# Kernel optimization log

Hardware: AMD Instinct MI355X
Metric: run time of the kernel (lower is better)

## Reference

```python
import jax, jax.numpy as jnp
import numpy as np

V, E, H, K, L, B = 32000, 512, 1024, 2048, 196, 256


def setup_inputs() -> dict:
    key = jax.random.key(0)
    ks = jax.random.split(key, 16)
    s = 0.02
    return {
        "inputs": jax.random.randint(ks[0], (B, 1), 0, V),
        "hidden": jax.random.normal(ks[1], (B, H), jnp.float32),
        "keys": jax.random.normal(ks[2], (B, L, K), jnp.float32),
        # embedding table
        "emb": jax.random.normal(ks[3], (V, E), jnp.float32) * s,
        # Bahdanau attention: Wq(hidden->H), Wk(keys_hidden->H), v(H->1)
        "Wq": jax.random.normal(ks[4], (H, H), jnp.float32) * s,
        "bq": jnp.zeros((H,), jnp.float32),
        "Wk": jax.random.normal(ks[5], (K, H), jnp.float32) * s,
        "bk": jnp.zeros((H,), jnp.float32),
        "v": jax.random.normal(ks[6], (H, 1), jnp.float32) * s,
        "bv": jnp.zeros((1,), jnp.float32),
        # fc_0: keys_hidden -> hidden
        "fc0_W": jax.random.normal(ks[7], (K, H), jnp.float32) * s,
        "fc0_b": jnp.zeros((H,), jnp.float32),
        # single-layer GRU, input dim E+H (PyTorch layout: [3H, in])
        "W_ih": jax.random.normal(ks[8], (3 * H, E + H), jnp.float32) * s,
        "W_hh": jax.random.normal(ks[9], (3 * H, H), jnp.float32) * s,
        "b_ih": jnp.zeros((3 * H,), jnp.float32),
        "b_hh": jnp.zeros((3 * H,), jnp.float32),
        # fc_1: hidden -> vocab
        "fc1_W": jax.random.normal(ks[10], (H, V), jnp.float32) * s,
        "fc1_b": jnp.zeros((V,), jnp.float32),
    }


def reference(inputs, hidden, keys, emb, Wq, bq, Wk, bk, v, bv,
              fc0_W, fc0_b, W_ih, W_hh, b_ih, b_hh, fc1_W, fc1_b):
    # embedding lookup: [B,1] -> [B,E] (single decode step)
    x = emb[inputs[:, 0]]
    # Bahdanau attention: score = v^T tanh(Wq q + Wk k)
    q = hidden @ Wq + bq                                   # [B,H]
    kproj = jnp.einsum('blk,kh->blh', keys, Wk) + bk        # [B,L,H]
    scores = jnp.tanh(q[:, None, :] + kproj) @ v + bv       # [B,L,1]
    weights = jax.nn.softmax(scores, axis=1)                # [B,L,1]
    context = jnp.sum(weights * keys, axis=1)               # [B,K]
    context = context @ fc0_W + fc0_b                       # [B,H]
    # one GRU step (PyTorch equations)
    rnn_in = jnp.concatenate([x, context], axis=-1)         # [B,E+H]
    gi = rnn_in @ W_ih.T + b_ih                             # [B,3H]
    gh = hidden @ W_hh.T + b_hh                             # [B,3H]
    ir, iz, i_n = jnp.split(gi, 3, axis=-1)
    hr, hz, h_n = jnp.split(gh, 3, axis=-1)
    r = jax.nn.sigmoid(ir + hr)
    z = jax.nn.sigmoid(iz + hz)
    n = jnp.tanh(i_n + r * h_n)
    h_new = (1.0 - z) * n + z * hidden                      # [B,H]
    logits = h_new @ fc1_W + fc1_b                          # [B,V]
    return logits, h_new, weights
```

## Files before the change

### kernel.cpp

```cpp
#include <hip/hip_runtime.h>
#include <cstdint>

#define DEVINL __device__ __forceinline__

typedef __attribute__((ext_vector_type(4))) float floatx4;
typedef __attribute__((ext_vector_type(8))) __bf16 bf16x8;
typedef __attribute__((ext_vector_type(8))) unsigned short ushortx8;
typedef __attribute__((ext_vector_type(4))) unsigned short ushortx4;

DEVINL unsigned short f2bf(float x) {
  unsigned int u = __float_as_uint(x);
  u += 0x7fffu + ((u >> 16) & 1u);
  return (unsigned short)(u >> 16);
}
DEVINL float bf2f(unsigned short u) { return __uint_as_float(((unsigned int)u) << 16); }

DEVINL float fast_tanh(float x) {
  return 1.0f - 2.0f / (__expf(2.0f * x) + 1.0f);
}

DEVINL void gload_lds16(const void* g, void* l) {
  __builtin_amdgcn_global_load_lds(
      (const __attribute__((address_space(1))) void*)g,
      (__attribute__((address_space(3))) void*)l, 16, 0, 0);
}

template <int EPI, bool ABF16, bool XSWZ>
__global__ __launch_bounds__(256) void gemm_bt(
    const float* __restrict__ Af, const unsigned short* __restrict__ Ab, int lda,
    const unsigned short* __restrict__ Bt, int ldb, int Kc,
    float* __restrict__ C, int ldc, int coloff, const float* __restrict__ bias,
    const float* __restrict__ qv, const float* __restrict__ bkv,
    const float* __restrict__ vvec, float* __restrict__ scores, int Lrows, int Hdim)
{
  __shared__ __align__(16) unsigned short As[128 * 32];
  __shared__ __align__(16) unsigned short Bs[128 * 32];

  const int tid  = threadIdx.x;
  const int wave = tid >> 6;
  const int lane = tid & 63;
  const int qd   = lane >> 4;
  const int lm   = lane & 15;
  const int wr   = wave >> 1;
  const int wc   = wave & 1;

  int bx = blockIdx.x, by = blockIdx.y;
  if (XSWZ) {
    const int id = by * 8 + bx;
    const int c = id >> 6, r = id & 63;
    by = c * 8 + (r & 7);
    bx = r >> 3;
  }
  const long n0 = (long)bx * 128;
  const long m0 = (long)by * 128;
  const long k0base = (long)blockIdx.z * Kc;

  floatx4 acc[4][4];
#pragma unroll
  for (int i = 0; i < 4; ++i)
#pragma unroll
    for (int j = 0; j < 4; ++j)
#pragma unroll
      for (int r = 0; r < 4; ++r) acc[i][j][r] = 0.0f;

  const int srow = lane >> 2;
  const int scg  = ((lane & 3) ^ ((lane >> 2) & 3) ^ (lane >> 4)) * 8;
  const int arow = tid >> 1;
  const int q0   = (tid & 1) * 2;
  const int sA   = ((arow & 3) ^ ((arow >> 2) & 3));
  const int fsw  = (qd ^ ((lm ^ (lm >> 2)) & 3)) * 8;

  const int nIter = Kc >> 5;
  for (int it = 0; it < nIter; ++it) {
    const long k0 = k0base + ((long)it << 5);
    {
      const unsigned short* bsrc = Bt + n0 * (size_t)ldb + k0;
#pragma unroll
      for (int q2 = 0; q2 < 2; ++q2) {
        const int rb = wave * 32 + q2 * 16;
        gload_lds16(bsrc + (size_t)(rb + srow) * ldb + scg, &Bs[rb * 32]);
      }
    }
    if (ABF16) {
      const unsigned short* asrc = Ab + m0 * (size_t)lda + k0;
#pragma unroll
      for (int q2 = 0; q2 < 2; ++q2) {
        const int rb = wave * 32 + q2 * 16;
        gload_lds16(asrc + (size_t)(rb + srow) * lda + scg, &As[rb * 32]);
      }
    } else {
      const float* ap = Af + (m0 + arow) * (size_t)lda + k0 + q0 * 8;
      floatx4 f0 = *(const floatx4*)(ap + 0);
      floatx4 f1 = *(const floatx4*)(ap + 4);
      floatx4 f2 = *(const floatx4*)(ap + 8);
      floatx4 f3 = *(const floatx4*)(ap + 12);
      ushortx8 u0, u1;
#pragma unroll
      for (int e = 0; e < 4; ++e) {
        u0[e]     = f2bf(f0[e]);
        u0[e + 4] = f2bf(f1[e]);
        u1[e]     = f2bf(f2[e]);
        u1[e + 4] = f2bf(f3[e]);
      }
      *(ushortx8*)&As[arow * 32 + (q0 ^ sA) * 8]       = u0;
      *(ushortx8*)&As[arow * 32 + ((q0 + 1) ^ sA) * 8] = u1;
    }
    __syncthreads();

    bf16x8 af[4], bfr[4];
#pragma unroll
    for (int i = 0; i < 4; ++i) {
      const int m = wr * 64 + i * 16 + lm;
      af[i] = *(const bf16x8*)&As[m * 32 + fsw];
    }
#pragma unroll
    for (int j = 0; j < 4; ++j) {
      const int n = wc * 64 + j * 16 + lm;
      bfr[j] = *(const bf16x8*)&Bs[n * 32 + fsw];
    }
#pragma unroll
    for (int i = 0; i < 4; ++i)
#pragma unroll
      for (int j = 0; j < 4; ++j)
        acc[i][j] = __builtin_amdgcn_mfma_f32_16x16x32_bf16(af[i], bfr[j], acc[i][j], 0, 0, 0);
    __syncthreads();
  }

  if (EPI == 0) {
#pragma unroll
    for (int j = 0; j < 4; ++j) {
      const long gc = n0 + wc * 64 + j * 16 + lm;
      const float bj = bias[gc];
#pragma unroll
      for (int i = 0; i < 4; ++i) {
        const long gr0 = m0 + wr * 64 + i * 16 + qd * 4;
#pragma unroll
        for (int r = 0; r < 4; ++r)
          C[(gr0 + r) * (size_t)ldc + coloff + gc] = acc[i][j][r] + bj;
      }
    }
  } else if (EPI == 2) {
#pragma unroll
    for (int j = 0; j < 4; ++j) {
      const long gc = n0 + wc * 64 + j * 16 + lm;
      const float bj = (blockIdx.z == 0) ? bias[gc] : 0.0f;
#pragma unroll
      for (int i = 0; i < 4; ++i) {
        const long gr0 = m0 + wr * 64 + i * 16 + qd * 4;
#pragma unroll
        for (int r = 0; r < 4; ++r)
          atomicAdd(&C[(gr0 + r) * (size_t)ldc + coloff + gc], acc[i][j][r] + bj);
      }
    }
  } else {
    float vj[4], bkj[4];
    int gcj[4];
#pragma unroll
    for (int j = 0; j < 4; ++j) {
      gcj[j] = (int)(n0 + wc * 64 + j * 16 + lm);
      vj[j]  = vvec[gcj[j]];
      bkj[j] = bkv[gcj[j]];
    }
    const int m0i = (int)m0;
#pragma unroll
    for (int i = 0; i < 4; ++i) {
#pragma unroll
      for (int r = 0; r < 4; ++r) {
        const int grow = m0i + wr * 64 + i * 16 + qd * 4 + r;
        int brow;
        if (Lrows == 196) brow = (int)((unsigned)(grow * 85599u) >> 24);
        else              brow = grow / Lrows;
        const float* qrow = qv + (size_t)brow * Hdim;
        float s = 0.0f;
#pragma unroll
        for (int j = 0; j < 4; ++j)
          s += fast_tanh(qrow[gcj[j]] + bkj[j] + acc[i][j][r]) * vj[j];
        s += __shfl_xor(s, 1, 64);
        s += __shfl_xor(s, 2, 64);
        s += __shfl_xor(s, 4, 64);
        s += __shfl_xor(s, 8, 64);
        if (lm == 0) atomicAdd(&scores[grow], s);
      }
    }
  }
}

__global__ void transpose_f32_bf16(const float* __restrict__ in,
                                   unsigned short* __restrict__ out, int R, int C) {
  __shared__ float tile[32][33];
  const int c0 = blockIdx.x * 32, r0 = blockIdx.y * 32;
  const int tx = threadIdx.x, ty = threadIdx.y;
#pragma unroll
  for (int yy = 0; yy < 4; ++yy)
    tile[ty + 8 * yy][tx] = in[(size_t)(r0 + ty + 8 * yy) * C + c0 + tx];
  __syncthreads();
#pragma unroll
  for (int yy = 0; yy < 4; ++yy)
    out[(size_t)(c0 + ty + 8 * yy) * R + r0 + tx] = f2bf(tile[tx][ty + 8 * yy]);
}

__global__ void convert_bf16(const float* __restrict__ in,
                             unsigned short* __restrict__ out, int n4) {
  const int idx = blockIdx.x * blockDim.x + threadIdx.x;
  if (idx < n4) {
    floatx4 f = *(const floatx4*)(in + 4 * (size_t)idx);
    ushortx4 u;
#pragma unroll
    for (int e = 0; e < 4; ++e) u[e] = f2bf(f[e]);
    *(ushortx4*)(out + 4 * (size_t)idx) = u;
  }
}

__global__ void gather_emb(const int* __restrict__ inputs, const float* __restrict__ emb,
                           float* __restrict__ rnn_in, int E, int ldr) {
  const int b = blockIdx.x, t = threadIdx.x;
  const int row = inputs[b];
  for (int e = t; e < E; e += 256)
    rnn_in[(size_t)b * ldr + e] = emb[(size_t)row * E + e];
}

__global__ __launch_bounds__(256) void softmax_w(
    const float* __restrict__ scores, const float* __restrict__ bv,
    float* __restrict__ weights, int L)
{
  __shared__ float red[8];
  const int b = blockIdx.x, t = threadIdx.x;
  const int wave = t >> 6;
  float s = (t < L) ? scores[(size_t)b * L + t] + bv[0] : -3.4e38f;
  float m = s;
  for (int o = 32; o > 0; o >>= 1) m = fmaxf(m, __shfl_xor(m, o, 64));
  if ((t & 63) == 0) red[wave] = m;
  __syncthreads();
  m = fmaxf(fmaxf(red[0], red[1]), fmaxf(red[2], red[3]));
  float e = (t < L) ? __expf(s - m) : 0.0f;
  float sum = e;
  for (int o = 32; o > 0; o >>= 1) sum += __shfl_xor(sum, o, 64);
  if ((t & 63) == 0) red[4 + wave] = sum;
  __syncthreads();
  sum = red[4] + red[5] + red[6] + red[7];
  if (t < L) weights[(size_t)b * L + t] = e / sum;
}

template <bool KB16>
__global__ __launch_bounds__(256) void context_k(
    const float* __restrict__ weights, const unsigned short* __restrict__ keys16,
    const float* __restrict__ keysf, float* __restrict__ context, int L, int K)
{
  __shared__ float w[256];
  const int b = blockIdx.x, t = threadIdx.x;
  if (t < L) w[t] = weights[(size_t)b * L + t];
  __syncthreads();
  const int col0 = blockIdx.y * 512 + t * 2;
  float a0 = 0.0f, a1 = 0.0f;
  if (KB16) {
    const unsigned short* kp = keys16 + (size_t)b * L * K + col0;
#pragma unroll 4
    for (int l = 0; l < L; ++l) {
      const unsigned int u = *(const unsigned int*)(kp + (size_t)l * K);
      a0 += w[l] * bf2f((unsigned short)(u & 0xffff));
      a1 += w[l] * bf2f((unsigned short)(u >> 16));
    }
  } else {
    const float* kp = keysf + (size_t)b * L * K + col0;
#pragma unroll 4
    for (int l = 0; l < L; ++l) {
      a0 += w[l] * kp[(size_t)l * K];
      a1 += w[l] * kp[(size_t)l * K + 1];
    }
  }
  context[(size_t)b * K + col0]     = a0;
  context[(size_t)b * K + col0 + 1] = a1;
}

__global__ void gru_kernel(const float* __restrict__ gi, const float* __restrict__ gh,
                           const float* __restrict__ hidden, float* __restrict__ hnew, int H) {
  const int idx = blockIdx.x * blockDim.x + threadIdx.x;
  const int b = idx / H, h = idx % H;
  const size_t base = (size_t)b * 3 * H;
  const float ir = gi[base + h], iz = gi[base + H + h], inn = gi[base + 2 * H + h];
  const float hr = gh[base + h], hz = gh[base + H + h], hn = gh[base + 2 * H + h];
  const float r = 1.0f / (1.0f + __expf(-(ir + hr)));
  const float z = 1.0f / (1.0f + __expf(-(iz + hz)));
  const float n = tanhf(inn + r * hn);
  const float hv = hidden[(size_t)b * H + h];
  hnew[(size_t)b * H + h] = (1.0f - z) * n + z * hv;
}

extern "C" void kernel_launch(void* const* d_in, const int* in_sizes, int n_in,
                              void* d_out, int out_size, void* d_ws, size_t ws_size,
                              hipStream_t stream) {
  constexpr int V = 32000, E = 512, H = 1024, KD = 2048, L = 196, B = 256;
  constexpr int G3 = 3 * H;
  constexpr int EH = E + H;

  const int*   inputs = (const int*)d_in[0];
  const float* hidden = (const float*)d_in[1];
  const float* keys   = (const float*)d_in[2];
  const float* emb    = (const float*)d_in[3];
  const float* Wq     = (const float*)d_in[4];
  const float* bq     = (const float*)d_in[5];
  const float* Wk     = (const float*)d_in[6];
  const float* bk     = (const float*)d_in[7];
  const float* vvec   = (const float*)d_in[8];
  const float* bv     = (const float*)d_in[9];
  const float* fc0_W  = (const float*)d_in[10];
  const float* fc0_b  = (const float*)d_in[11];
  const float* W_ih   = (const float*)d_in[12];
  const float* W_hh   = (const float*)d_in[13];
  const float* b_ih   = (const float*)d_in[14];
  const float* b_hh   = (const float*)d_in[15];
  const float* fc1_W  = (const float*)d_in[16];
  const float* fc1_b  = (const float*)d_in[17];

  float* logits  = (float*)d_out;
  float* hnew    = logits + (size_t)B * V;
  float* weights = hnew + (size_t)B * H;

  char* ws = (char*)d_ws;
  size_t off = 0;
  auto bump = [&off](size_t bytes) {
    size_t p = off;
    off += (bytes + 255) & ~(size_t)255;
    return p;
  };
  unsigned short* WqT   = (unsigned short*)(ws + bump((size_t)H * H * 2));
  unsigned short* WkT   = (unsigned short*)(ws + bump((size_t)H * KD * 2));
  unsigned short* fc0T  = (unsigned short*)(ws + bump((size_t)H * KD * 2));
  unsigned short* fc1T  = (unsigned short*)(ws + bump((size_t)V * H * 2));
  unsigned short* Wih16 = (unsigned short*)(ws + bump((size_t)G3 * EH * 2));
  unsigned short* Whh16 = (unsigned short*)(ws + bump((size_t)G3 * H * 2));
  float* qbuf    = (float*)(ws + bump((size_t)B * H * 4));
  float* scoresb = (float*)(ws + bump((size_t)B * L * 4));
  float* context = (float*)(ws + bump((size_t)B * KD * 4));
  float* rnn_in  = (float*)(ws + bump((size_t)B * EH * 4));
  float* gi      = (float*)(ws + bump((size_t)B * G3 * 4));
  float* gh      = (float*)(ws + bump((size_t)B * G3 * 4));
  unsigned short* keys16 = (unsigned short*)(ws + bump((size_t)B * L * KD * 2));
  const bool useK16 = (off <= ws_size);

  hipMemsetAsync(scoresb, 0, (size_t)B * L * 4, stream);
  hipMemsetAsync(qbuf, 0, (size_t)B * H * 4, stream);
  hipMemsetAsync(rnn_in, 0, (size_t)B * EH * 4, stream);
  hipMemsetAsync(gi, 0, (size_t)B * G3 * 4, stream);
  hipMemsetAsync(gh, 0, (size_t)B * G3 * 4, stream);

  const dim3 tb(32, 8);
  transpose_f32_bf16<<<dim3(H / 32, H / 32), tb, 0, stream>>>(Wq, WqT, H, H);
  transpose_f32_bf16<<<dim3(H / 32, KD / 32), tb, 0, stream>>>(Wk, WkT, KD, H);
  transpose_f32_bf16<<<dim3(H / 32, KD / 32), tb, 0, stream>>>(fc0_W, fc0T, KD, H);
  transpose_f32_bf16<<<dim3(V / 32, H / 32), tb, 0, stream>>>(fc1_W, fc1T, H, V);
  convert_bf16<<<(G3 * EH / 4 + 255) / 256, 256, 0, stream>>>(W_ih, Wih16, G3 * EH / 4);
  convert_bf16<<<(G3 * H / 4 + 255) / 256, 256, 0, stream>>>(W_hh, Whh16, G3 * H / 4);
  if (useK16) {
    const int n4 = B * L * KD / 4;
    convert_bf16<<<(n4 + 255) / 256, 256, 0, stream>>>(keys, keys16, n4);
  }

  gather_emb<<<B, 256, 0, stream>>>(inputs, emb, rnn_in, E, EH);

  gemm_bt<2, false, false><<<dim3(H / 128, B / 128, 4), 256, 0, stream>>>(
      hidden, nullptr, H, WqT, H, H / 4, qbuf, H, 0, bq,
      nullptr, nullptr, nullptr, nullptr, 0, 0);

  if (useK16)
    gemm_bt<1, true, true><<<dim3(H / 128, (B * L) / 128, 1), 256, 0, stream>>>(
        nullptr, keys16, KD, WkT, KD, KD, nullptr, 0, 0, nullptr,
        qbuf, bk, vvec, scoresb, L, H);
  else
    gemm_bt<1, false, true><<<dim3(H / 128, (B * L) / 128, 1), 256, 0, stream>>>(
        keys, nullptr, KD, WkT, KD, KD, nullptr, 0, 0, nullptr,
        qbuf, bk, vvec, scoresb, L, H);

  softmax_w<<<B, 256, 0, stream>>>(scoresb, bv, weights, L);

  if (useK16)
    context_k<true><<<dim3(B, KD / 512), 256, 0, stream>>>(weights, keys16, nullptr,
                                                           context, L, KD);
  else
    context_k<false><<<dim3(B, KD / 512), 256, 0, stream>>>(weights, nullptr, keys,
                                                            context, L, KD);

  gemm_bt<2, false, false><<<dim3(H / 128, B / 128, 4), 256, 0, stream>>>(
      context, nullptr, KD, fc0T, KD, KD / 4, rnn_in, EH, E, fc0_b,
      nullptr, nullptr, nullptr, nullptr, 0, 0);

  gemm_bt<2, false, false><<<dim3(G3 / 128, B / 128, 4), 256, 0, stream>>>(
      rnn_in, nullptr, EH, Wih16, EH, EH / 4, gi, G3, 0, b_ih,
      nullptr, nullptr, nullptr, nullptr, 0, 0);

  gemm_bt<2, false, false><<<dim3(G3 / 128, B / 128, 4), 256, 0, stream>>>(
      hidden, nullptr, H, Whh16, H, H / 4, gh, G3, 0, b_hh,
      nullptr, nullptr, nullptr, nullptr, 0, 0);

  gru_kernel<<<(B * H) / 256, 256, 0, stream>>>(gi, gh, hidden, hnew, H);

  gemm_bt<0, false, false><<<dim3(V / 128, B / 128, 1), 256, 0, stream>>>(
      hnew, nullptr, H, fc1T, H, H, logits, V, 0, fc1_b,
      nullptr, nullptr, nullptr, nullptr, 0, 0);
}
```

Baseline: 1.267 ms.

## Replace key-projection score GEMM with 256x256 eight-phase pipelined MFMA kernel

Adds a dedicated 512-thread kernel for the dominant keys·Wk GEMM with the fused tanh/v score epilogue. It uses 256x256 tiles, double-buffered LDS filled by direct global-to-LDS loads, XOR-swizzled LDS reads, and an eight-phase schedule that interleaves loads with MFMA blocks and raises wave priority around them. The goal is more data reuse per tile and better overlap of memory traffic with matrix math than the previous 128x128 kernel. In exchange it uses a large LDS footprint (128KB) that limits occupancy, hardcodes K=2048, L=196 and H=1024 (batch row is computed by a magic multiply), and still sums scores with atomics.

```diff
diff --git a/kernel.cpp b/kernel.cpp
--- a/kernel.cpp
+++ b/kernel.cpp
@@ -23,6 +23,151 @@
   __builtin_amdgcn_global_load_lds(
       (const __attribute__((address_space(1))) void*)g,
       (__attribute__((address_space(3))) void*)l, 16, 0, 0);
+}
+
+#define SBAR()                          \
+  __builtin_amdgcn_sched_barrier(0);    \
+  __builtin_amdgcn_s_barrier();         \
+  __builtin_amdgcn_sched_barrier(0);
+
+__global__ __launch_bounds__(512) void gemm_scores_8ph(
+    const unsigned short* __restrict__ A, const unsigned short* __restrict__ B,
+    const float* __restrict__ qv, const float* __restrict__ bkv,
+    const float* __restrict__ vvec, float* __restrict__ scores)
+{
+  constexpr int KSH = 2048;
+  constexpr int NT  = 32;
+  __shared__ __align__(16) unsigned short lds[2 * 4 * 8192];
+
+  const int tid  = threadIdx.x;
+  const int w    = tid >> 6;
+  const int lane = tid & 63;
+  const int qd = lane >> 4, lm = lane & 15;
+  const int wm = w >> 2;
+  const int wn = w & 3;
+
+  const int n0 = blockIdx.x * 256;
+  const int m0 = blockIdx.y * 256;
+
+  const int off0 = (w * 16 + 0 + (lane >> 3)) * KSH + ((lane & 7) ^ (lane >> 3)) * 8;
+  const int off1 = (w * 16 + 8 + (lane >> 3)) * KSH + ((lane & 7) ^ (lane >> 3)) * 8;
+
+  const unsigned short* srcu[4] = {
+      A + (size_t)m0 * KSH, A + (size_t)(m0 + 128) * KSH,
+      B + (size_t)n0 * KSH, B + (size_t)(n0 + 128) * KSH};
+
+#define STAGE(u, tt)                                                          \
+  {                                                                           \
+    const unsigned short* s_ = srcu[u] + (tt) * 64;                           \
+    unsigned short* d_ = &lds[(((tt) & 1) * 4 + (u)) * 8192 + w * 1024];      \
+    gload_lds16(s_ + off0, d_);                                               \
+    gload_lds16(s_ + off1, d_ + 512);                                         \
+  }
+
+  const int fswz = lm & 7;
+#define READ_A(mh)                                                            \
+  _Pragma("unroll") for (int mf = 0; mf < 4; ++mf)                            \
+  _Pragma("unroll") for (int kk = 0; kk < 2; ++kk)                            \
+      af[mf][kk] = *(const bf16x8*)&Ab_[((mh)*64 + mf * 16 + lm) * 64 +       \
+                                        ((kk * 4 + qd) ^ fswz) * 8];
+
+#define READ_B(nh, dst)                                                       \
+  _Pragma("unroll") for (int nf = 0; nf < 2; ++nf)                            \
+  _Pragma("unroll") for (int kk = 0; kk < 2; ++kk)                            \
+      dst[nf][kk] = *(const bf16x8*)&Bb_[(bro + (nh)*32 + nf * 16 + lm) * 64 +\
+                                         ((kk * 4 + qd) ^ fswz) * 8];
+
+#define QUAD(mh, nh, bsrc)                                                    \
+  _Pragma("unroll") for (int mf = 0; mf < 4; ++mf)                            \
+  _Pragma("unroll") for (int nf = 0; nf < 2; ++nf)                            \
+  _Pragma("unroll") for (int kk = 0; kk < 2; ++kk)                            \
+      acc[(mh)*4 + mf][(nh)*2 + nf] = __builtin_amdgcn_mfma_f32_16x16x32_bf16(\
+          af[mf][kk], bsrc[nf][kk], acc[(mh)*4 + mf][(nh)*2 + nf], 0, 0, 0);
+
+  floatx4 acc[8][4];
+#pragma unroll
+  for (int i = 0; i < 8; ++i)
+#pragma unroll
+    for (int j = 0; j < 4; ++j)
+#pragma unroll
+      for (int r = 0; r < 4; ++r) acc[i][j][r] = 0.0f;
+
+  STAGE(0, 0) STAGE(1, 0) STAGE(2, 0) STAGE(3, 0)
+  STAGE(2, 1) STAGE(3, 1) STAGE(0, 1)
+  asm volatile("s_waitcnt vmcnt(6)" ::: "memory");
+  SBAR();
+
+  const int bro = (wn & 1) * 64;
+  bf16x8 af[4][2], b0[2][2], b1[2][2];
+
+#pragma unroll 2
+  for (int t = 0; t < NT; ++t) {
+    const unsigned short* Ab_ = &lds[(t & 1) * 32768 + wm * 8192];
+    const unsigned short* Bb_ = &lds[(t & 1) * 32768 + (2 + (wn >> 1)) * 8192];
+    READ_A(0)
+    READ_B(0, b0)
+    if (t + 1 < NT) STAGE(1, t + 1)
+    SBAR();
+    __builtin_amdgcn_s_setprio(1);
+    QUAD(0, 0, b0)
+    __builtin_amdgcn_s_setprio(0);
+    SBAR();
+    READ_B(1, b1)
+    SBAR();
+    __builtin_amdgcn_s_setprio(1);
+    QUAD(0, 1, b1)
+    __builtin_amdgcn_s_setprio(0);
+    SBAR();
+    READ_A(1)
+    if (t + 2 < NT) STAGE(2, t + 2)
+    SBAR();
+    __builtin_amdgcn_s_setprio(1);
+    QUAD(1, 0, b0)
+    __builtin_amdgcn_s_setprio(0);
+    SBAR();
+    if (t + 2 < NT) { STAGE(3, t + 2) STAGE(0, t + 2) }
+    SBAR();
+    __builtin_amdgcn_s_setprio(1);
+    QUAD(1, 1, b1)
+    __builtin_amdgcn_s_setprio(0);
+    if (t + 2 < NT) {
+      asm volatile("s_waitcnt vmcnt(6)" ::: "memory");
+    } else if (t + 1 < NT) {
+      asm volatile("s_waitcnt vmcnt(0)" ::: "memory");
+    }
+    SBAR();
+  }
+
+  float vj[4], bkj[4];
+  int gcj[4];
+#pragma unroll
+  for (int nf = 0; nf < 4; ++nf) {
+    gcj[nf] = n0 + wn * 64 + nf * 16 + lm;
+    vj[nf]  = vvec[gcj[nf]];
+    bkj[nf] = bkv[gcj[nf]];
+  }
+#pragma unroll
+  for (int mf = 0; mf < 8; ++mf) {
+#pragma unroll
+    for (int r = 0; r < 4; ++r) {
+      const int grow = m0 + wm * 128 + mf * 16 + qd * 4 + r;
+      const int brow = (int)((unsigned)(grow * 85599u) >> 24);
+      const float* qrow = qv + (size_t)brow * 1024;
+      float s = 0.0f;
+#pragma unroll
+      for (int nf = 0; nf < 4; ++nf)
+        s += fast_tanh(qrow[gcj[nf]] + bkj[nf] + acc[mf][nf][r]) * vj[nf];
+      s += __shfl_xor(s, 1, 64);
+      s += __shfl_xor(s, 2, 64);
+      s += __shfl_xor(s, 4, 64);
+      s += __shfl_xor(s, 8, 64);
+      if (lm == 0) atomicAdd(&scores[grow], s);
+    }
+  }
+#undef STAGE
+#undef READ_A
+#undef READ_B
+#undef QUAD
 }
 
 template <int EPI, bool ABF16, bool XSWZ>
@@ -363,9 +508,8 @@
       nullptr, nullptr, nullptr, nullptr, 0, 0);
 
   if (useK16)
-    gemm_bt<1, true, true><<<dim3(H / 128, (B * L) / 128, 1), 256, 0, stream>>>(
-        nullptr, keys16, KD, WkT, KD, KD, nullptr, 0, 0, nullptr,
-        qbuf, bk, vvec, scoresb, L, H);
+    gemm_scores_8ph<<<dim3((H) / 256, (B * L) / 256, 1), 512, 0, stream>>>(
+        keys16, WkT, qbuf, bk, vvec, scoresb);
   else
     gemm_bt<1, false, true><<<dim3(H / 128, (B * L) / 128, 1), 256, 0, stream>>>(
         keys, nullptr, KD, WkT, KD, KD, nullptr, 0, 0, nullptr,
```

Result: faster. 1.204 ms (-5.0%).
